# Performance work log

Measured on AMD Instinct MI355X. Metric: run time of the kernel, lower is better.

Reference implementation:

```python
import jax, jax.numpy as jnp
import numpy as np

MS_KS = 9
C = 256
BN_EPS = 1e-5


def setup_inputs() -> dict:
    key = jax.random.key(0)
    k1, k2, k3 = jax.random.split(key, 3)
    p2_r = jax.random.normal(k1, (2, C, 64, 128), dtype=jnp.float32)
    conv_w = jax.random.normal(k2, (C, C, 1, MS_KS), dtype=jnp.float32) * 0.02
    conv1_w = jax.random.normal(k3, (1, C, 1, 1), dtype=jnp.float32) * 0.05
    bn_gamma = jnp.ones((1,), jnp.float32)
    bn_beta = jnp.zeros((1,), jnp.float32)
    return dict(p2_r=p2_r, conv_w=conv_w, conv1_w=conv1_w,
                bn_gamma=bn_gamma, bn_beta=bn_beta)


def _scnn_pass(x, M):
    # x: [b,c,h,w]. Each step applies conv(1,ms_ks) to a width-1 column with
    # zero padding ms_ks//2 -> only the center tap contributes, i.e. a 256x256
    # channel matmul per column, followed by relu and residual add.
    cols = jnp.moveaxis(x, 3, 0)  # [w,b,c,h]
    def step(carry, col):
        new = col + jax.nn.relu(jnp.einsum('oc,bch->boh', M, carry))
        return new, new
    _, outs = jax.lax.scan(step, cols[0], cols[1:])
    outs = jnp.concatenate([cols[:1], outs], axis=0)[::-1]  # mirrors out[::-1]
    return jnp.moveaxis(outs, 0, 3)


def _upsample_bilinear_ac(x, factor=4):
    # F.interpolate(mode='bilinear', align_corners=True)
    b, c, h, w = x.shape
    Ho, Wo = factor * h, factor * w
    ys = jnp.arange(Ho, dtype=x.dtype) * ((h - 1) / (Ho - 1))
    xs = jnp.arange(Wo, dtype=x.dtype) * ((w - 1) / (Wo - 1))
    y0 = jnp.floor(ys).astype(jnp.int32)
    y1 = jnp.minimum(y0 + 1, h - 1)
    wy = (ys - y0.astype(x.dtype))[None, None, :, None]
    rows = x[:, :, y0, :] * (1 - wy) + x[:, :, y1, :] * wy  # [b,c,Ho,w]
    x0 = jnp.floor(xs).astype(jnp.int32)
    x1 = jnp.minimum(x0 + 1, w - 1)
    wx = (xs - x0.astype(x.dtype))[None, None, None, :]
    return rows[:, :, :, x0] * (1 - wx) + rows[:, :, :, x1] * wx


def reference(p2_r, conv_w, conv1_w, bn_gamma, bn_beta):
    M = conv_w[:, :, 0, MS_KS // 2]  # center tap, [c_out, c_in]
    x = _scnn_pass(p2_r, M)                     # reverse=False
    x = _scnn_pass(x[:, :, :, ::-1], M)         # reverse=True (slices[::-1])
    x = _upsample_bilinear_ac(x, 4)             # [b,256,4h,4w]
    x = jnp.einsum('oc,bchw->bohw', conv1_w[:, :, 0, 0], x)  # 1x1 conv -> 1 ch
    # BatchNorm2d(1), training-mode batch statistics (biased variance)
    mean = jnp.mean(x, axis=(0, 2, 3), keepdims=True)
    var = jnp.mean((x - mean) ** 2, axis=(0, 2, 3), keepdims=True)
    x = (x - mean) * jax.lax.rsqrt(var + BN_EPS)
    x = x * bn_gamma[None, :, None, None] + bn_beta[None, :, None, None]
    return jax.nn.sigmoid(x)
```

## Files before the change

kernel.cpp:

```cpp
#include <hip/hip_runtime.h>


typedef _Float16 f16x8 __attribute__((ext_vector_type(8)));
typedef _Float16 f16x4 __attribute__((ext_vector_type(4)));
typedef float    f32x4 __attribute__((ext_vector_type(4)));

static __device__ __forceinline__ int xchg_pair(int x) {
#if __has_builtin(__builtin_amdgcn_update_dpp)
  return __builtin_amdgcn_update_dpp(x, x, 0xB1, 0xF, 0xF, true);
#else
  return __shfl_xor(x, 1, 64);
#endif
}

extern "C" __global__ void k_extract(const float* __restrict__ convw,
                                     _Float16* __restrict__ Md) {
  int q = blockIdx.x * 256 + threadIdx.x;
  float4 v = ((const float4*)convw)[q];
  float vv[4] = {v.x, v.y, v.z, v.w};
  int f = q * 4;
#pragma unroll
  for (int e = 0; e < 4; ++e) {
    int flat = f + e;
    if (flat % 9 == 4) Md[flat / 9] = (_Float16)vv[e];
  }
}

struct SM {
  _Float16 cy[2][256];
  _Float16 pad0[32];
  _Float16 cz[2][256];
  _Float16 pad1[32];
  float    cbuf[2][16][256];
  float    sp[128][20];
};

extern "C" __global__ void __launch_bounds__(256, 1)
k_scan(const float* __restrict__ p2, const _Float16* __restrict__ Md,
       const float* __restrict__ conv1, float* __restrict__ sout,
       float* __restrict__ stats, unsigned int* __restrict__ cnt) {
  __shared__ SM sm;
  const int tid  = threadIdx.x;
  const int l    = tid & 63;
  const int r    = tid >> 6;
  const int col  = l & 15;
  const int quad = l >> 4;
  const int b    = blockIdx.x >> 6;
  const int h    = blockIdx.x & 63;

  if (blockIdx.x == 0 && tid == 0) { stats[0] = 0.f; stats[1] = 0.f; *cnt = 0u; }

  const bool isY = (col == 0);
  const bool isZ = (col == 1);
  const int  mq  = r * 64 + quad * 4;

  const float* pbase = p2 + (size_t)b * 2097152 + (size_t)h * 128;

  {
    const f32x4* g = (const f32x4*)(pbase + (size_t)tid * 8192);
    f32x4 g0 = g[0], g1 = g[1], g2 = g[2], g3 = g[3];
#pragma unroll
    for (int j = 0; j < 4; ++j) {
      sm.cbuf[0][j][tid]      = g0[j];
      sm.cbuf[0][4 + j][tid]  = g1[j];
      sm.cbuf[0][8 + j][tid]  = g2[j];
      sm.cbuf[0][12 + j][tid] = g3[j];
    }
  }

  f16x8 A[4][8];
#pragma unroll
  for (int t = 0; t < 4; ++t)
#pragma unroll
    for (int ch = 0; ch < 8; ++ch)
      A[t][ch] = *(const f16x8*)(Md + (size_t)(r * 64 + t * 16 + col) * 256 +
                                 ch * 32 + quad * 8);

  float vvf[16];
#pragma unroll
  for (int t = 0; t < 4; ++t) {
    f32x4 vt = *(const f32x4*)(conv1 + mq + t * 16);
#pragma unroll
    for (int i = 0; i < 4; ++i) vvf[t * 4 + i] = vt[i];
  }
  __syncthreads();

  {
    f32x4 c0[4];
#pragma unroll
    for (int t = 0; t < 4; ++t)
      c0[t] = *(const f32x4*)(&sm.cbuf[0][0][mq + t * 16]);
    if (isY) {
#pragma unroll
      for (int t = 0; t < 4; ++t) {
        f16x4 p;
#pragma unroll
        for (int i = 0; i < 4; ++i) p[i] = (_Float16)c0[t][i];
        *(f16x4*)(sm.cy[0] + mq + t * 16) = p;
        *(f16x4*)(sm.cz[0] + mq + t * 16) = p;
      }
    }
    if (isZ) {
      float p = 0.f;
#pragma unroll
      for (int t = 0; t < 4; ++t)
#pragma unroll
        for (int i = 0; i < 4; ++i) p += vvf[t * 4 + i] * c0[t][i];
      sm.sp[0][r * 4 + quad] = p;
    }
  }
  __syncthreads();

  const _Float16* selA = ((l & 1) ? sm.cz[0] : sm.cy[0]) + quad * 8;
  const _Float16* selB = ((l & 1) ? sm.cz[1] : sm.cy[1]) + quad * 8;

#define STEP(W, SELP, WY, WZ, DOSTAGE)                                         \
  do {                                                                         \
    f32x4 g0, g1, g2, g3;                                                      \
    bool stg = (DOSTAGE) && (((W) & 15) == 1) && ((W) < 113);                  \
    int t1 = ((W) >> 4) + 1;                                                   \
    if (stg) {                                                                 \
      const f32x4* g = (const f32x4*)(pbase + (size_t)tid * 8192 + t1 * 16);   \
      g0 = g[0]; g1 = g[1]; g2 = g[2]; g3 = g[3];                              \
    }                                                                          \
    f16x8 B[8];                                                                \
    _Pragma("unroll")                                                          \
    for (int ch = 0; ch < 8; ++ch)                                             \
      B[ch] = *(const f16x8*)((SELP) + ch * 32);                               \
    const float* cb = &sm.cbuf[((W) >> 4) & 1][(W) & 15][0];                   \
    f32x4 cr[4];                                                               \
    _Pragma("unroll")                                                          \
    for (int t = 0; t < 4; ++t)                                                \
      cr[t] = *(const f32x4*)(cb + mq + t * 16);     \
    f32x4 acc[4];                                                              \
    _Pragma("unroll")                                                          \
    for (int t = 0; t < 4; ++t) {                                              \
      f32x4 p0 = {0.f, 0.f, 0.f, 0.f}, p1 = {0.f, 0.f, 0.f, 0.f};             \
      p0 = __builtin_amdgcn_mfma_f32_16x16x32_f16(A[t][0], B[0], p0, 0, 0, 0); \
      p1 = __builtin_amdgcn_mfma_f32_16x16x32_f16(A[t][4], B[4], p1, 0, 0, 0); \
      p0 = __builtin_amdgcn_mfma_f32_16x16x32_f16(A[t][1], B[1], p0, 0, 0, 0); \
      p1 = __builtin_amdgcn_mfma_f32_16x16x32_f16(A[t][5], B[5], p1, 0, 0, 0); \
      p0 = __builtin_amdgcn_mfma_f32_16x16x32_f16(A[t][2], B[2], p0, 0, 0, 0); \
      p1 = __builtin_amdgcn_mfma_f32_16x16x32_f16(A[t][6], B[6], p1, 0, 0, 0); \
      p0 = __builtin_amdgcn_mfma_f32_16x16x32_f16(A[t][3], B[3], p0, 0, 0, 0); \
      p1 = __builtin_amdgcn_mfma_f32_16x16x32_f16(A[t][7], B[7], p1, 0, 0, 0); \
      acc[t] = p0 + p1;                                                        \
    }                                                                          \
                       \
    f16x4 yh[4], ys[4];                                                        \
    _Pragma("unroll")                                                          \
    for (int t = 0; t < 4; ++t) {                                              \
      _Pragma("unroll")                                                        \
      for (int i = 0; i < 4; ++i)                                              \
        yh[t][i] = (_Float16)(cr[t][i] + fmaxf(acc[t][i], 0.f));               \
      int2 u = __builtin_bit_cast(int2, yh[t]);                                \
      u.x = xchg_pair(u.x); u.y = xchg_pair(u.y);                              \
      ys[t] = __builtin_bit_cast(f16x4, u);      \
    }                                                                          \
    if (isY) {                                                                 \
      _Pragma("unroll")                                                        \
      for (int t = 0; t < 4; ++t)                                              \
        *(f16x4*)((WY) + mq + t * 16) = yh[t];                                 \
    }                                                                          \
    if (isZ) {                                                                 \
      float p = 0.f;                                                           \
      _Pragma("unroll")                                                        \
      for (int t = 0; t < 4; ++t) {                                            \
        f16x4 zh;                                                              \
        _Pragma("unroll")                                                      \
        for (int i = 0; i < 4; ++i) {                                          \
          float z = (float)ys[t][i] + fmaxf(acc[t][i], 0.f);                   \
          zh[i] = (_Float16)z;                                                 \
          p += vvf[t * 4 + i] * z;                                             \
        }                                                                      \
        *(f16x4*)((WZ) + mq + t * 16) = zh;                                    \
      }                                                                        \
      sm.sp[(W)][r * 4 + quad] = p;                                            \
    }                                                                          \
    if (stg) {                                                                 \
      int bs = t1 & 1;                                                         \
      _Pragma("unroll")                                                        \
      for (int j = 0; j < 4; ++j) {                                            \
        sm.cbuf[bs][j][tid]      = g0[j];                                      \
        sm.cbuf[bs][4 + j][tid]  = g1[j];                                      \
        sm.cbuf[bs][8 + j][tid]  = g2[j];                                      \
        sm.cbuf[bs][12 + j][tid] = g3[j];                                      \
      }                                                                        \
    }                                                                          \
    __syncthreads();                                                           \
  } while (0)

#pragma unroll 1
  for (int w = 1; w < 127; w += 2) {
    STEP(w,     selA, sm.cy[1], sm.cz[1], 1);
    STEP(w + 1, selB, sm.cy[0], sm.cz[0], 0);
  }
  STEP(127, selA, sm.cy[1], sm.cz[1], 0);
#undef STEP

  if (tid < 128) {
    const f32x4* q = (const f32x4*)(sm.sp[tid]);
    f32x4 q0 = q[0], q1 = q[1], q2 = q[2], q3 = q[3];
    float s = q0[0] + q0[1] + q0[2] + q0[3] + q1[0] + q1[1] + q1[2] + q1[3] +
              q2[0] + q2[1] + q2[2] + q2[3] + q3[0] + q3[1] + q3[2] + q3[3];
    sout[(blockIdx.x << 7) + (127 - tid)] = s;
  }
}

static __device__ __forceinline__ float bilin(const float* __restrict__ s,
                                              int idx) {
  int bb  = idx >> 17;
  int rem = idx & 131071;
  int ho  = rem >> 9;
  int wo  = rem & 511;
  const float SY = 63.0f / 255.0f, SX = 127.0f / 511.0f;
  float fy = (float)ho * SY;
  int y0 = (int)fy; int y1 = min(y0 + 1, 63); float wy = fy - (float)y0;
  float fx = (float)wo * SX;
  int x0 = (int)fx; int x1 = min(x0 + 1, 127); float wx = fx - (float)x0;
  const float* sb = s + bb * 8192;
  float cA = sb[y0 * 128 + x0] * (1.f - wy) + sb[y1 * 128 + x0] * wy;
  float cB = sb[y0 * 128 + x1] * (1.f - wy) + sb[y1 * 128 + x1] * wy;
  return cA * (1.f - wx) + cB * wx;
}

extern "C" __global__ void __launch_bounds__(256, 1)
k_statsnorm(const float* __restrict__ s, float* __restrict__ stats,
            unsigned int* __restrict__ cnt, const float* __restrict__ gamma,
            const float* __restrict__ beta, float* __restrict__ out) {
  int tid  = threadIdx.x;
  int base = blockIdx.x * 1024 + tid;
  float u[4];
  float sum = 0.f, ssq = 0.f;
#pragma unroll
  for (int i = 0; i < 4; ++i) {
    u[i] = bilin(s, base + i * 256);
    sum += u[i]; ssq += u[i] * u[i];
  }
#pragma unroll
  for (int off = 32; off > 0; off >>= 1) {
    sum += __shfl_xor(sum, off, 64);
    ssq += __shfl_xor(ssq, off, 64);
  }
  __shared__ float ls[4], lq[4];
  int wv = tid >> 6;
  if ((tid & 63) == 0) { ls[wv] = sum; lq[wv] = ssq; }
  __syncthreads();
  if (tid == 0) {
    float bsum = ls[0] + ls[1] + ls[2] + ls[3];
    float bssq = lq[0] + lq[1] + lq[2] + lq[3];
    __hip_atomic_fetch_add(&stats[0], bsum, __ATOMIC_RELAXED, __HIP_MEMORY_SCOPE_AGENT);
    __hip_atomic_fetch_add(&stats[1], bssq, __ATOMIC_RELAXED, __HIP_MEMORY_SCOPE_AGENT);
    __hip_atomic_fetch_add(cnt, 1u, __ATOMIC_RELEASE, __HIP_MEMORY_SCOPE_AGENT);
    while (__hip_atomic_load(cnt, __ATOMIC_ACQUIRE, __HIP_MEMORY_SCOPE_AGENT) < 256u)
      __builtin_amdgcn_s_sleep(8);
  }
  __syncthreads();
  float s0 = __hip_atomic_load(&stats[0], __ATOMIC_RELAXED, __HIP_MEMORY_SCOPE_AGENT);
  float s1 = __hip_atomic_load(&stats[1], __ATOMIC_RELAXED, __HIP_MEMORY_SCOPE_AGENT);
  const float invN = 1.f / 262144.f;
  float mean  = s0 * invN;
  float var   = s1 * invN - mean * mean;
  float scale = rsqrtf(var + 1e-5f) * gamma[0];
  float bias  = beta[0] - mean * scale;
#pragma unroll
  for (int i = 0; i < 4; ++i) {
    float x = u[i] * scale + bias;
    out[base + i * 256] = 1.f / (1.f + __expf(-x));
  }
}

extern "C" void kernel_launch(void* const* d_in, const int* in_sizes, int n_in,
                              void* d_out, int out_size, void* d_ws, size_t ws_size,
                              hipStream_t stream) {
  const float* p2    = (const float*)d_in[0];
  const float* convw = (const float*)d_in[1];
  const float* conv1 = (const float*)d_in[2];
  const float* gamma = (const float*)d_in[3];
  const float* beta  = (const float*)d_in[4];
  float* out = (float*)d_out;

  char* ws = (char*)d_ws;
  float*        s     = (float*)ws;
  float*        stats = (float*)(ws + 65536);
  unsigned int* cnt   = (unsigned int*)(ws + 65544);
  _Float16*     Md    = (_Float16*)(ws + 65792);

  hipLaunchKernelGGL(k_extract,   dim3(576), dim3(256), 0, stream, convw, Md);
  hipLaunchKernelGGL(k_scan,      dim3(128), dim3(256), 0, stream,
                     p2, Md, conv1, s, stats, cnt);
  hipLaunchKernelGGL(k_statsnorm, dim3(256), dim3(256), 0, stream,
                     s, stats, cnt, gamma, beta, out);
}
```

Baseline: 196.6 us.

## Pack two scan chains per block and use packed f16 epilogue math

Each 512-thread block now runs two independent (batch, row) recurrence chains, each with its own shared-memory set, so the grid is halved to 64 blocks. The staged input columns are stored as f16 instead of f32. The per-step residual, ReLU and conv1 dot product now use packed half arithmetic, with pkrtz conversion and fdot2. The aim is a shorter serial per-step epilogue and less LDS traffic, and letting the two chains hide each other's latency on one CU. In exchange, the residual path loses precision, and a single __syncthreads now couples both chains.

```diff
diff --git a/kernel.cpp b/kernel.cpp
--- a/kernel.cpp
+++ b/kernel.cpp
@@ -3,8 +3,19 @@
 
 typedef _Float16 f16x8 __attribute__((ext_vector_type(8)));
 typedef _Float16 f16x4 __attribute__((ext_vector_type(4)));
+typedef _Float16 h2    __attribute__((ext_vector_type(2)));
 typedef float    f32x4 __attribute__((ext_vector_type(4)));
 
+static __device__ __forceinline__ h2 pkrtz(float a, float b) {
+  return __builtin_bit_cast(h2, __builtin_amdgcn_cvt_pkrtz(a, b));
+}
+static __device__ __forceinline__ float fdot2(h2 a, h2 b, float c) {
+#if __has_builtin(__builtin_amdgcn_fdot2)
+  return __builtin_amdgcn_fdot2(a, b, c, false);
+#else
+  return c + (float)a.x * (float)b.x + (float)a.y * (float)b.y;
+#endif
+}
 static __device__ __forceinline__ int xchg_pair(int x) {
 #if __has_builtin(__builtin_amdgcn_update_dpp)
   return __builtin_amdgcn_update_dpp(x, x, 0xB1, 0xF, 0xF, true);
@@ -26,45 +37,49 @@
   }
 }
 
-struct SM {
+struct SMG {
   _Float16 cy[2][256];
   _Float16 pad0[32];
   _Float16 cz[2][256];
   _Float16 pad1[32];
-  float    cbuf[2][16][256];
-  float    sp[128][20];
+  _Float16 cbuf[2][16][256];
+  float    sp[128][24];
 };
 
-extern "C" __global__ void __launch_bounds__(256, 1)
+extern "C" __global__ void __launch_bounds__(512, 2)
 k_scan(const float* __restrict__ p2, const _Float16* __restrict__ Md,
        const float* __restrict__ conv1, float* __restrict__ sout,
        float* __restrict__ stats, unsigned int* __restrict__ cnt) {
-  __shared__ SM sm;
+  __shared__ SMG smg[2];
   const int tid  = threadIdx.x;
+  const int g    = tid >> 8;
+  const int tg   = tid & 255;
   const int l    = tid & 63;
-  const int r    = tid >> 6;
+  const int rr   = tg >> 6;
   const int col  = l & 15;
   const int quad = l >> 4;
-  const int b    = blockIdx.x >> 6;
-  const int h    = blockIdx.x & 63;
+  const int cidx = (blockIdx.x << 1) | g;
+  const int bb   = cidx >> 6;
+  const int hh   = cidx & 63;
 
   if (blockIdx.x == 0 && tid == 0) { stats[0] = 0.f; stats[1] = 0.f; *cnt = 0u; }
 
+  SMG& sm = smg[g];
   const bool isY = (col == 0);
   const bool isZ = (col == 1);
-  const int  mq  = r * 64 + quad * 4;
-
-  const float* pbase = p2 + (size_t)b * 2097152 + (size_t)h * 128;
+  const int  mq  = rr * 64 + quad * 4;
+
+  const float* pbase = p2 + (size_t)bb * 2097152 + (size_t)hh * 128;
 
   {
-    const f32x4* g = (const f32x4*)(pbase + (size_t)tid * 8192);
-    f32x4 g0 = g[0], g1 = g[1], g2 = g[2], g3 = g[3];
+    const f32x4* gp = (const f32x4*)(pbase + (size_t)tg * 8192);
+    f32x4 g0 = gp[0], g1 = gp[1], g2 = gp[2], g3 = gp[3];
 #pragma unroll
     for (int j = 0; j < 4; ++j) {
-      sm.cbuf[0][j][tid]      = g0[j];
-      sm.cbuf[0][4 + j][tid]  = g1[j];
-      sm.cbuf[0][8 + j][tid]  = g2[j];
-      sm.cbuf[0][12 + j][tid] = g3[j];
+      sm.cbuf[0][j][tg]      = (_Float16)g0[j];
+      sm.cbuf[0][4 + j][tg]  = (_Float16)g1[j];
+      sm.cbuf[0][8 + j][tg]  = (_Float16)g2[j];
+      sm.cbuf[0][12 + j][tg] = (_Float16)g3[j];
     }
   }
 
@@ -73,40 +88,42 @@
   for (int t = 0; t < 4; ++t)
 #pragma unroll
     for (int ch = 0; ch < 8; ++ch)
-      A[t][ch] = *(const f16x8*)(Md + (size_t)(r * 64 + t * 16 + col) * 256 +
+      A[t][ch] = *(const f16x8*)(Md + (size_t)(rr * 64 + t * 16 + col) * 256 +
                                  ch * 32 + quad * 8);
 
-  float vvf[16];
+  h2 vv01[4], vv23[4];
 #pragma unroll
   for (int t = 0; t < 4; ++t) {
     f32x4 vt = *(const f32x4*)(conv1 + mq + t * 16);
-#pragma unroll
-    for (int i = 0; i < 4; ++i) vvf[t * 4 + i] = vt[i];
+    vv01[t] = pkrtz(vt[0], vt[1]);
+    vv23[t] = pkrtz(vt[2], vt[3]);
   }
   __syncthreads();
 
   {
-    f32x4 c0[4];
-#pragma unroll
-    for (int t = 0; t < 4; ++t)
-      c0[t] = *(const f32x4*)(&sm.cbuf[0][0][mq + t * 16]);
+    h2 c01[4], c23[4];
+#pragma unroll
+    for (int t = 0; t < 4; ++t) {
+      const h2* cp = (const h2*)(&sm.cbuf[0][0][mq + t * 16]);
+      c01[t] = cp[0]; c23[t] = cp[1];
+    }
     if (isY) {
 #pragma unroll
       for (int t = 0; t < 4; ++t) {
-        f16x4 p;
-#pragma unroll
-        for (int i = 0; i < 4; ++i) p[i] = (_Float16)c0[t][i];
-        *(f16x4*)(sm.cy[0] + mq + t * 16) = p;
-        *(f16x4*)(sm.cz[0] + mq + t * 16) = p;
+        int2 u = make_int2(__builtin_bit_cast(int, c01[t]),
+                           __builtin_bit_cast(int, c23[t]));
+        *(int2*)(sm.cy[0] + mq + t * 16) = u;
+        *(int2*)(sm.cz[0] + mq + t * 16) = u;
       }
     }
     if (isZ) {
       float p = 0.f;
 #pragma unroll
-      for (int t = 0; t < 4; ++t)
-#pragma unroll
-        for (int i = 0; i < 4; ++i) p += vvf[t * 4 + i] * c0[t][i];
-      sm.sp[0][r * 4 + quad] = p;
+      for (int t = 0; t < 4; ++t) {
+        p = fdot2(vv01[t], c01[t], p);
+        p = fdot2(vv23[t], c23[t], p);
+      }
+      sm.sp[0][rr * 4 + quad] = p;
     }
   }
   __syncthreads();
@@ -117,21 +134,16 @@
 #define STEP(W, SELP, WY, WZ, DOSTAGE)                                         \
   do {                                                                         \
     f32x4 g0, g1, g2, g3;                                                      \
-    bool stg = (DOSTAGE) && (((W) & 15) == 1) && ((W) < 113);                  \
+    bool stg = (DOSTAGE) && (((W) & 15) == 1) && ((W) < 98);                   \
     int t1 = ((W) >> 4) + 1;                                                   \
     if (stg) {                                                                 \
-      const f32x4* g = (const f32x4*)(pbase + (size_t)tid * 8192 + t1 * 16);   \
-      g0 = g[0]; g1 = g[1]; g2 = g[2]; g3 = g[3];                              \
+      const f32x4* gp = (const f32x4*)(pbase + (size_t)tg * 8192 + t1 * 16);   \
+      g0 = gp[0]; g1 = gp[1]; g2 = gp[2]; g3 = gp[3];                          \
     }                                                                          \
     f16x8 B[8];                                                                \
     _Pragma("unroll")                                                          \
     for (int ch = 0; ch < 8; ++ch)                                             \
       B[ch] = *(const f16x8*)((SELP) + ch * 32);                               \
-    const float* cb = &sm.cbuf[((W) >> 4) & 1][(W) & 15][0];                   \
-    f32x4 cr[4];                                                               \
-    _Pragma("unroll")                                                          \
-    for (int t = 0; t < 4; ++t)                                                \
-      cr[t] = *(const f32x4*)(cb + mq + t * 16);     \
     f32x4 acc[4];                                                              \
     _Pragma("unroll")                                                          \
     for (int t = 0; t < 4; ++t) {                                              \
@@ -146,47 +158,39 @@
       p1 = __builtin_amdgcn_mfma_f32_16x16x32_f16(A[t][7], B[7], p1, 0, 0, 0); \
       acc[t] = p0 + p1;                                                        \
     }                                                                          \
-                       \
-    f16x4 yh[4], ys[4];                                                        \
-    _Pragma("unroll")                                                          \
-    for (int t = 0; t < 4; ++t) {                                              \
-      _Pragma("unroll")                                                        \
-      for (int i = 0; i < 4; ++i)                                              \
-        yh[t][i] = (_Float16)(cr[t][i] + fmaxf(acc[t][i], 0.f));               \
-      int2 u = __builtin_bit_cast(int2, yh[t]);                                \
-      u.x = xchg_pair(u.x); u.y = xchg_pair(u.y);                              \
-      ys[t] = __builtin_bit_cast(f16x4, u);      \
-    }                                                                          \
-    if (isY) {                                                                 \
-      _Pragma("unroll")                                                        \
-      for (int t = 0; t < 4; ++t)                                              \
-        *(f16x4*)((WY) + mq + t * 16) = yh[t];                                 \
-    }                                                                          \
-    if (isZ) {                                                                 \
-      float p = 0.f;                                                           \
-      _Pragma("unroll")                                                        \
-      for (int t = 0; t < 4; ++t) {                                            \
-        f16x4 zh;                                                              \
-        _Pragma("unroll")                                                      \
-        for (int i = 0; i < 4; ++i) {                                          \
-          float z = (float)ys[t][i] + fmaxf(acc[t][i], 0.f);                   \
-          zh[i] = (_Float16)z;                                                 \
-          p += vvf[t * 4 + i] * z;                                             \
-        }                                                                      \
-        *(f16x4*)((WZ) + mq + t * 16) = zh;                                    \
-      }                                                                        \
-      sm.sp[(W)][r * 4 + quad] = p;                                            \
-    }                                                                          \
     if (stg) {                                                                 \
       int bs = t1 & 1;                                                         \
       _Pragma("unroll")                                                        \
       for (int j = 0; j < 4; ++j) {                                            \
-        sm.cbuf[bs][j][tid]      = g0[j];                                      \
-        sm.cbuf[bs][4 + j][tid]  = g1[j];                                      \
-        sm.cbuf[bs][8 + j][tid]  = g2[j];                                      \
-        sm.cbuf[bs][12 + j][tid] = g3[j];                                      \
+        sm.cbuf[bs][j][tg]      = (_Float16)g0[j];                             \
+        sm.cbuf[bs][4 + j][tg]  = (_Float16)g1[j];                             \
+        sm.cbuf[bs][8 + j][tg]  = (_Float16)g2[j];                             \
+        sm.cbuf[bs][12 + j][tg] = (_Float16)g3[j];                             \
       }                                                                        \
     }                                                                          \
+    const _Float16* cb = &sm.cbuf[((W) >> 4) & 1][(W) & 15][0];                \
+    float p = 0.f;                                                             \
+    _Pragma("unroll")                                                          \
+    for (int t = 0; t < 4; ++t) {                                              \
+      const h2* cp = (const h2*)(cb + mq + t * 16);         \
+      h2 c01 = cp[0], c23 = cp[1];                                             \
+      h2 rm01 = pkrtz(fmaxf(acc[t][0], 0.f), fmaxf(acc[t][1], 0.f));           \
+      h2 rm23 = pkrtz(fmaxf(acc[t][2], 0.f), fmaxf(acc[t][3], 0.f));           \
+      h2 yh01 = c01 + rm01, yh23 = c23 + rm23;               \
+      int u0 = __builtin_bit_cast(int, yh01), u1 = __builtin_bit_cast(int, yh23);\
+      if (isY) *(int2*)((WY) + mq + t * 16) = make_int2(u0, u1);               \
+      h2 ys01 = __builtin_bit_cast(h2, xchg_pair(u0));                         \
+      h2 ys23 = __builtin_bit_cast(h2, xchg_pair(u1));                         \
+      h2 zh01 = ys01 + rm01, zh23 = ys23 + rm23;                               \
+      if (isZ) {                                                               \
+        *(int2*)((WZ) + mq + t * 16) =                                         \
+            make_int2(__builtin_bit_cast(int, zh01),                           \
+                      __builtin_bit_cast(int, zh23));                          \
+        p = fdot2(vv01[t], zh01, p);                                           \
+        p = fdot2(vv23[t], zh23, p);                                           \
+      }                                                                        \
+    }                                                                          \
+    if (isZ) sm.sp[(W)][rr * 4 + quad] = p;                                    \
     __syncthreads();                                                           \
   } while (0)
 
@@ -198,12 +202,12 @@
   STEP(127, selA, sm.cy[1], sm.cz[1], 0);
 #undef STEP
 
-  if (tid < 128) {
-    const f32x4* q = (const f32x4*)(sm.sp[tid]);
+  if (tg < 128) {
+    const f32x4* q = (const f32x4*)(sm.sp[tg]);
     f32x4 q0 = q[0], q1 = q[1], q2 = q[2], q3 = q[3];
     float s = q0[0] + q0[1] + q0[2] + q0[3] + q1[0] + q1[1] + q1[2] + q1[3] +
               q2[0] + q2[1] + q2[2] + q2[3] + q3[0] + q3[1] + q3[2] + q3[3];
-    sout[(blockIdx.x << 7) + (127 - tid)] = s;
+    sout[(cidx << 7) + (127 - tg)] = s;
   }
 }
 
@@ -287,7 +291,7 @@
   _Float16*     Md    = (_Float16*)(ws + 65792);
 
   hipLaunchKernelGGL(k_extract,   dim3(576), dim3(256), 0, stream, convw, Md);
-  hipLaunchKernelGGL(k_scan,      dim3(128), dim3(256), 0, stream,
+  hipLaunchKernelGGL(k_scan,      dim3(64),  dim3(512), 0, stream,
                      p2, Md, conv1, s, stats, cnt);
   hipLaunchKernelGGL(k_statsnorm, dim3(256), dim3(256), 0, stream,
                      s, stats, cnt, gamma, beta, out);
```

Result: slower. 216.8 us (+10.3%).
